# Kernel tuning notes

Hardware: AMD Instinct MI355X
Metric: run time of the kernel (lower is better)

## Reference

```python
import jax, jax.numpy as jnp
import numpy as np

OUT_F, IN_F, BLOCK, RANK = 8192, 8192, 32, 16
B, S = 4, 256
Q_ZERO = 128.0      # symmetric int8-style zero point for the Q8_0-like quants
LORA_SCALE = 2.0    # patch alpha applied by the patch function


def setup_inputs() -> dict:
    key = jax.random.key(0)
    k1, k2, k3, k4, k5, k6 = jax.random.split(key, 6)
    x = jax.random.normal(k1, (B, S, IN_F), dtype=jnp.float32)
    # block-quantized weight: int quants in [0,256) and per-block scales
    q_int = jax.random.randint(k2, (OUT_F, IN_F // BLOCK, BLOCK), 0, 256, dtype=jnp.int32)
    scales = jax.random.uniform(k3, (OUT_F, IN_F // BLOCK), dtype=jnp.float32) * 0.02
    lora_A = jax.random.normal(k4, (RANK, IN_F), dtype=jnp.float32) * 0.02
    lora_B = jax.random.normal(k5, (OUT_F, RANK), dtype=jnp.float32) * 0.02
    bias = jax.random.normal(k6, (OUT_F,), dtype=jnp.float32)
    return {"x": x, "q_int": q_int, "scales": scales,
            "lora_A": lora_A, "lora_B": lora_B, "bias": bias}


def reference(x, q_int, scales, lora_A, lora_B, bias):
    # --- get_weight(): dequantize GGML block-quantized tensor ---
    # w[o, b, e] = (q[o, b, e] - 128) * scale[o, b]
    w = (q_int.astype(jnp.float32) - Q_ZERO) * scales[:, :, None]   # [out, in//BLOCK, BLOCK]
    w = w.reshape(OUT_F, IN_F)                                      # [out, in]
    # --- apply patch function (LoRA add) ---
    w = w + LORA_SCALE * (lora_B @ lora_A)                          # [out, in]
    # --- cast_bias_weight + F.linear ---
    w = w.astype(x.dtype)
    y = jnp.einsum('bsi,oi->bso', x, w) + bias.astype(x.dtype)      # [B, S, out]
    return y
```

## Files before the change

### kernel.cpp

```cpp
#include <hip/hip_runtime.h>
#include <hip/hip_bf16.h>
#include <stdint.h>

#define OUT_F 8192
#define IN_F  8192
#define RANK  16
#define M_TOT 1024
#define BM 128
#define BN 128
#define BK 64
#define NK (IN_F / BK)
#define SCB (IN_F / 32)

typedef __bf16 bf16x8 __attribute__((ext_vector_type(8)));
typedef float  f32x4  __attribute__((ext_vector_type(4)));

static __device__ __forceinline__ uint32_t pack_bf16(float lo, float hi) {
    uint32_t a = __builtin_bit_cast(uint32_t, lo);
    uint32_t b = __builtin_bit_cast(uint32_t, hi);
    return ((a + 0x8000u) >> 16) | ((b + 0x8000u) & 0xffff0000u);
}

__global__ __launch_bounds__(256) void prep_kernel(
    const float* __restrict__ x, const int* __restrict__ q,
    uint2* __restrict__ xb2, uint32_t* __restrict__ qu32,
    float* __restrict__ t)
{
    const int gid = blockIdx.x * 256 + threadIdx.x;
    if (gid < M_TOT * RANK) t[gid] = 0.f;

    const float4* x4 = (const float4*)x;
#pragma unroll
    for (int j = 0; j < 4; ++j) {
        const int i = gid + j * 524288;
        const float4 v = x4[i];
        uint2 p;
        p.x = pack_bf16(v.x, v.y);
        p.y = pack_bf16(v.z, v.w);
        xb2[i] = p;
    }

    const int4* q4 = (const int4*)q;
#pragma unroll 8
    for (int k = 0; k < 32; ++k) {
        const size_t i = (size_t)gid + (size_t)k * 524288;
        const int4 a = q4[i];
        qu32[i] = (uint32_t)a.x | ((uint32_t)a.y << 8) |
                  ((uint32_t)a.z << 16) | ((uint32_t)a.w << 24);
    }
}

__global__ __launch_bounds__(256) void convert_kernel(
    const float* __restrict__ x, uint2* __restrict__ xb2, float* __restrict__ t)
{
    const int tid = threadIdx.x, b = blockIdx.x;
    if (b < 64) t[b * 256 + tid] = 0.f;
    const float4* x4 = (const float4*)x;
    const int base = b * 256 + tid;
#pragma unroll
    for (int j = 0; j < 8; ++j) {
        const int i = base + j * 262144;
        const float4 v = x4[i];
        uint2 p;
        p.x = pack_bf16(v.x, v.y);
        p.y = pack_bf16(v.z, v.w);
        xb2[i] = p;
    }
}

__global__ __launch_bounds__(256) void lora_t_kernel(
    const uint16_t* __restrict__ xb, const float* __restrict__ lora_A,
    float* __restrict__ t)
{
    const int b = blockIdx.x;
    const int mt = b >> 6, ks = b & 63;
    const int tid = threadIdx.x, wave = tid >> 6, lane = tid & 63;
    const int fr = lane & 15, quad = lane >> 4;
    const int m = mt * 64 + wave * 16 + fr;
    const int k0 = ks * 128 + quad * 8;

    f32x4 acc = {0.f, 0.f, 0.f, 0.f};
    const uint16_t* xr = xb + (size_t)m * IN_F + k0;
    const float* ar = lora_A + (size_t)fr * IN_F + k0;

#pragma unroll
    for (int s = 0; s < 4; ++s) {
        const bf16x8 af = *(const bf16x8*)(xr + s * 32);
        const float4 a0 = *(const float4*)(ar + s * 32);
        const float4 a1 = *(const float4*)(ar + s * 32 + 4);
        bf16x8 bfr;
        uint32_t* bp = (uint32_t*)&bfr;
        bp[0] = pack_bf16(a0.x, a0.y); bp[1] = pack_bf16(a0.z, a0.w);
        bp[2] = pack_bf16(a1.x, a1.y); bp[3] = pack_bf16(a1.z, a1.w);
        acc = __builtin_amdgcn_mfma_f32_16x16x32_bf16(af, bfr, acc, 0, 0, 0);
    }
    const int mout = mt * 64 + wave * 16 + quad * 4;
#pragma unroll
    for (int r = 0; r < 4; ++r)
        atomicAdd(&t[(size_t)(mout + r) * RANK + fr], acc[r]);
}

#define GEMM_STEP_U(KT, P, CUR, NXT)                                           \
    {                                                                          \
        const int ktn = ((KT) + 2) & (NK - 1);                                 \
        _Pragma("unroll")                                                      \
        for (int j = 0; j < 8; ++j) {                                          \
            const int row = qrow + 16 * j;                                     \
            qv[(P) ^ 1][j] = *(const uint32_t*)(qbase + (size_t)row * IN_F + ktn * BK); \
            sc[(P) ^ 1][j] = scales[(size_t)(n0 + row) * SCB + ktn * 2 + qhi]; \
        }                                                                      \
        const int kta = ((KT) + 1) & (NK - 1);                                 \
        _Pragma("unroll")                                                      \
        for (int i = 0; i < 4; ++i) {                                          \
            __builtin_amdgcn_global_load_lds(                                  \
                (const __attribute__((address_space(1))) uint32_t*)(xsrc + (size_t)kta * BK + (size_t)i * 8 * IN_F), \
                (__attribute__((address_space(3))) uint32_t*)(&xs[NXT][(wave * 32 + i * 8) * BK]), \
                16, 0, 0);                                                     \
        }                                                                      \
        _Pragma("unroll")                                                      \
        for (int j = 0; j < 8; ++j) {                                          \
            const float s = sc[P][j];                                          \
            const float c = -128.f * s;                                        \
            const uint32_t qq = qv[P][j];                                      \
            uint2 pk;                                                          \
            pk.x = pack_bf16(fmaf((float)(qq & 0xffu), s, c),                  \
                             fmaf((float)((qq >> 8) & 0xffu), s, c));          \
            pk.y = pack_bf16(fmaf((float)((qq >> 16) & 0xffu), s, c),          \
                             fmaf((float)(qq >> 24), s, c));                   \
            *(uint2*)(&wt[NXT][(qrow + 16 * j) * BK + wpos]) = pk;             \
        }                                                                      \
        _Pragma("unroll")                                                      \
        for (int kk = 0; kk < BK; kk += 32) {                                  \
            bf16x8 af[4], bfr[4];                                              \
            const int pp = (((kk >> 3) + quad) ^ (fr & 7)) * 8;                \
            _Pragma("unroll")                                                  \
            for (int i = 0; i < 4; ++i)                                        \
                af[i] = *(const bf16x8*)(&xs[CUR][(wm * 64 + i * 16 + fr) * BK + pp]); \
            _Pragma("unroll")                                                  \
            for (int j = 0; j < 4; ++j)                                        \
                bfr[j] = *(const bf16x8*)(&wt[CUR][(wn * 64 + j * 16 + fr) * BK + pp]); \
            _Pragma("unroll")                                                  \
            for (int i = 0; i < 4; ++i)                                        \
                _Pragma("unroll")                                              \
                for (int j = 0; j < 4; ++j)                                    \
                    acc[i][j] = __builtin_amdgcn_mfma_f32_16x16x32_bf16(af[i], bfr[j], acc[i][j], 0, 0, 0); \
        }                                                                      \
        __syncthreads();                                                       \
    }

__global__ __launch_bounds__(256, 2) void gemm_u8_kernel(
    const uint16_t* __restrict__ xb,
    const uint8_t*  __restrict__ qu8,
    const float*    __restrict__ scales,
    const float*    __restrict__ t,
    const float*    __restrict__ loraB,
    const float*    __restrict__ bias,
    float*          __restrict__ out)
{
    __shared__ __align__(16) uint16_t xs[2][BM * BK];
    __shared__ __align__(16) uint16_t wt[2][BN * BK];

    const int bx    = blockIdx.x;
    const int mtile = bx >> 6;
    const int ntile = bx & 63;
    const int m0 = mtile * BM;
    const int n0 = ntile * BN;

    const int tid  = threadIdx.x;
    const int wave = tid >> 6;
    const int lane = tid & 63;
    const int wm = wave & 1, wn = wave >> 1;
    const int fr = lane & 15;
    const int quad = lane >> 4;

    const int qrow  = tid >> 4;
    const int qcol4 = (tid & 15) * 4;
    const int qhi   = (tid >> 3) & 1;
    const int wpos = ((((tid >> 1) & 7) ^ (qrow & 7)) * 8) + (tid & 1) * 4;

    const uint8_t* qbase = qu8 + (size_t)n0 * IN_F + qcol4;

    f32x4 acc[4][4];
    const f32x4 z = {0.f, 0.f, 0.f, 0.f};
#pragma unroll
    for (int i = 0; i < 4; ++i)
#pragma unroll
        for (int j = 0; j < 4; ++j) acc[i][j] = z;

    uint32_t qv[2][8];
    float    sc[2][8];

#pragma unroll
    for (int j = 0; j < 8; ++j) {
        const int row = qrow + 16 * j;
        qv[0][j] = *(const uint32_t*)(qbase + (size_t)row * IN_F);
        sc[0][j] = scales[(size_t)(n0 + row) * SCB + qhi];
    }

    {
        if (tid < 128) {
            const int row = tid, s = row & 7;
            const float4* tp = (const float4*)(t + (size_t)(m0 + row) * RANK);
            const float4 v0 = tp[0], v1 = tp[1], v2 = tp[2], v3 = tp[3];
            uint32_t vals[8];
            vals[0] = pack_bf16(v0.x, v0.y); vals[1] = pack_bf16(v0.z, v0.w);
            vals[2] = pack_bf16(v1.x, v1.y); vals[3] = pack_bf16(v1.z, v1.w);
            vals[4] = pack_bf16(v2.x, v2.y); vals[5] = pack_bf16(v2.z, v2.w);
            vals[6] = pack_bf16(v3.x, v3.y); vals[7] = pack_bf16(v3.z, v3.w);
            uint32_t* dst = (uint32_t*)(&xs[0][row * BK]);
#pragma unroll
            for (int c = 0; c < 8; ++c) {
                const int p = (c ^ s) * 4;
                if (c < 2) {
                    dst[p + 0] = vals[c * 4 + 0]; dst[p + 1] = vals[c * 4 + 1];
                    dst[p + 2] = vals[c * 4 + 2]; dst[p + 3] = vals[c * 4 + 3];
                } else {
                    dst[p + 0] = 0; dst[p + 1] = 0; dst[p + 2] = 0; dst[p + 3] = 0;
                }
            }
        } else {
            const int row = tid - 128, s = row & 7;
            const float4* bp = (const float4*)(loraB + (size_t)(n0 + row) * RANK);
            const float4 v0 = bp[0], v1 = bp[1], v2 = bp[2], v3 = bp[3];
            uint32_t vals[8];
            vals[0] = pack_bf16(2.f * v0.x, 2.f * v0.y); vals[1] = pack_bf16(2.f * v0.z, 2.f * v0.w);
            vals[2] = pack_bf16(2.f * v1.x, 2.f * v1.y); vals[3] = pack_bf16(2.f * v1.z, 2.f * v1.w);
            vals[4] = pack_bf16(2.f * v2.x, 2.f * v2.y); vals[5] = pack_bf16(2.f * v2.z, 2.f * v2.w);
            vals[6] = pack_bf16(2.f * v3.x, 2.f * v3.y); vals[7] = pack_bf16(2.f * v3.z, 2.f * v3.w);
            uint32_t* dst = (uint32_t*)(&wt[0][row * BK]);
#pragma unroll
            for (int c = 0; c < 8; ++c) {
                const int p = (c ^ s) * 4;
                if (c < 2) {
                    dst[p + 0] = vals[c * 4 + 0]; dst[p + 1] = vals[c * 4 + 1];
                    dst[p + 2] = vals[c * 4 + 2]; dst[p + 3] = vals[c * 4 + 3];
                } else {
                    dst[p + 0] = 0; dst[p + 1] = 0; dst[p + 2] = 0; dst[p + 3] = 0;
                }
            }
        }
        __syncthreads();
        const int pp = (quad ^ (fr & 7)) * 8;
        bf16x8 af[4], bfr[4];
#pragma unroll
        for (int i = 0; i < 4; ++i)
            af[i] = *(const bf16x8*)(&xs[0][(wm * 64 + i * 16 + fr) * BK + pp]);
#pragma unroll
        for (int j = 0; j < 4; ++j)
            bfr[j] = *(const bf16x8*)(&wt[0][(wn * 64 + j * 16 + fr) * BK + pp]);
#pragma unroll
        for (int i = 0; i < 4; ++i)
#pragma unroll
            for (int j = 0; j < 4; ++j)
                acc[i][j] = __builtin_amdgcn_mfma_f32_16x16x32_bf16(af[i], bfr[j], acc[i][j], 0, 0, 0);
        __syncthreads();
    }

    const int xrow   = wave * 32 + (lane >> 3);
    const int xchunk = (lane & 7) ^ (lane >> 3);
    const uint16_t* xsrc = xb + (size_t)(m0 + xrow) * IN_F + xchunk * 8;

#pragma unroll
    for (int i = 0; i < 4; ++i) {
        __builtin_amdgcn_global_load_lds(
            (const __attribute__((address_space(1))) uint32_t*)(xsrc + (size_t)i * 8 * IN_F),
            (__attribute__((address_space(3))) uint32_t*)(&xs[0][(wave * 32 + i * 8) * BK]),
            16, 0, 0);
    }
#pragma unroll
    for (int j = 0; j < 8; ++j) {
        const float s = sc[0][j];
        const float c = -128.f * s;
        const uint32_t qq = qv[0][j];
        uint2 pk;
        pk.x = pack_bf16(fmaf((float)(qq & 0xffu), s, c),
                         fmaf((float)((qq >> 8) & 0xffu), s, c));
        pk.y = pack_bf16(fmaf((float)((qq >> 16) & 0xffu), s, c),
                         fmaf((float)(qq >> 24), s, c));
        *(uint2*)(&wt[0][(qrow + 16 * j) * BK + wpos]) = pk;
    }
#pragma unroll
    for (int j = 0; j < 8; ++j) {
        const int row = qrow + 16 * j;
        qv[0][j] = *(const uint32_t*)(qbase + (size_t)row * IN_F + 1 * BK);
        sc[0][j] = scales[(size_t)(n0 + row) * SCB + 2 + qhi];
    }
    __syncthreads();

    for (int kt = 0; kt < NK; kt += 2) {
        GEMM_STEP_U(kt,     0, 0, 1);
        GEMM_STEP_U(kt + 1, 1, 1, 0);
    }

#pragma unroll
    for (int j = 0; j < 4; ++j) {
        const int col = n0 + wn * 64 + j * 16 + fr;
        const float bv = bias[col];
#pragma unroll
        for (int i = 0; i < 4; ++i) {
            const int rbase = m0 + wm * 64 + i * 16 + quad * 4;
#pragma unroll
            for (int r = 0; r < 4; ++r)
                out[(size_t)(rbase + r) * OUT_F + col] = acc[i][j][r] + bv;
        }
    }
}

#define GEMM_STEP_L(KT, P, CUR, NXT)                                           \
    {                                                                          \
        const int ktn = ((KT) + 2) & (NK - 1);                                 \
        _Pragma("unroll")                                                      \
        for (int j = 0; j < 8; ++j) {                                          \
            const int row = qrow + 16 * j;                                     \
            qv[(P) ^ 1][j] = *(const int4*)(qbase + (size_t)row * IN_F + ktn * BK); \
            sc[(P) ^ 1][j] = scales[(size_t)(n0 + row) * SCB + ktn * 2 + qhi]; \
        }                                                                      \
        const int kta = ((KT) + 1) & (NK - 1);                                 \
        _Pragma("unroll")                                                      \
        for (int i = 0; i < 4; ++i) {                                          \
            __builtin_amdgcn_global_load_lds(                                  \
                (const __attribute__((address_space(1))) uint32_t*)(xsrc + (size_t)kta * BK + (size_t)i * 8 * IN_F), \
                (__attribute__((address_space(3))) uint32_t*)(&xs[NXT][(wave * 32 + i * 8) * BK]), \
                16, 0, 0);                                                     \
        }                                                                      \
        _Pragma("unroll")                                                      \
        for (int j = 0; j < 8; ++j) {                                          \
            const float s = sc[P][j];                                          \
            const float c = -128.f * s;                                        \
            const int4 qq = qv[P][j];                                          \
            uint2 pk;                                                          \
            pk.x = pack_bf16(fmaf((float)qq.x, s, c), fmaf((float)qq.y, s, c)); \
            pk.y = pack_bf16(fmaf((float)qq.z, s, c), fmaf((float)qq.w, s, c)); \
            *(uint2*)(&wt[NXT][(qrow + 16 * j) * BK + wpos]) = pk;             \
        }                                                                      \
        _Pragma("unroll")                                                      \
        for (int kk = 0; kk < BK; kk += 32) {                                  \
            bf16x8 af[4], bfr[4];                                              \
            const int pp = (((kk >> 3) + quad) ^ (fr & 7)) * 8;                \
            _Pragma("unroll")                                                  \
            for (int i = 0; i < 4; ++i)                                        \
                af[i] = *(const bf16x8*)(&xs[CUR][(wm * 64 + i * 16 + fr) * BK + pp]); \
            _Pragma("unroll")                                                  \
            for (int j = 0; j < 4; ++j)                                        \
                bfr[j] = *(const bf16x8*)(&wt[CUR][(wn * 64 + j * 16 + fr) * BK + pp]); \
            _Pragma("unroll")                                                  \
            for (int i = 0; i < 4; ++i)                                        \
                _Pragma("unroll")                                              \
                for (int j = 0; j < 4; ++j)                                    \
                    acc[i][j] = __builtin_amdgcn_mfma_f32_16x16x32_bf16(af[i], bfr[j], acc[i][j], 0, 0, 0); \
        }                                                                      \
        __syncthreads();                                                       \
    }

__global__ __launch_bounds__(256, 2) void gemm_kernel(
    const uint16_t* __restrict__ xb,
    const int*      __restrict__ q,
    const float*    __restrict__ scales,
    const float*    __restrict__ t,
    const float*    __restrict__ loraB,
    const float*    __restrict__ bias,
    float*          __restrict__ out)
{
    __shared__ __align__(16) uint16_t xs[2][BM * BK];
    __shared__ __align__(16) uint16_t wt[2][BN * BK];

    const int bx    = blockIdx.x;
    const int mtile = bx >> 6;
    const int ntile = bx & 63;
    const int m0 = mtile * BM;
    const int n0 = ntile * BN;

    const int tid  = threadIdx.x;
    const int wave = tid >> 6;
    const int lane = tid & 63;
    const int wm = wave & 1, wn = wave >> 1;
    const int fr = lane & 15;
    const int quad = lane >> 4;

    const int qrow  = tid >> 4;
    const int qcol4 = (tid & 15) * 4;
    const int qhi   = (tid >> 3) & 1;
    const int wpos = ((((tid >> 1) & 7) ^ (qrow & 7)) * 8) + (tid & 1) * 4;

    const int* qbase = q + (size_t)n0 * IN_F + qcol4;

    f32x4 acc[4][4];
    const f32x4 z = {0.f, 0.f, 0.f, 0.f};
#pragma unroll
    for (int i = 0; i < 4; ++i)
#pragma unroll
        for (int j = 0; j < 4; ++j) acc[i][j] = z;

    int4  qv[2][8];
    float sc[2][8];

#pragma unroll
    for (int j = 0; j < 8; ++j) {
        const int row = qrow + 16 * j;
        qv[0][j] = *(const int4*)(qbase + (size_t)row * IN_F);
        sc[0][j] = scales[(size_t)(n0 + row) * SCB + qhi];
    }

    {
        if (tid < 128) {
            const int row = tid, s = row & 7;
            const float4* tp = (const float4*)(t + (size_t)(m0 + row) * RANK);
            const float4 v0 = tp[0], v1 = tp[1], v2 = tp[2], v3 = tp[3];
            uint32_t vals[8];
            vals[0] = pack_bf16(v0.x, v0.y); vals[1] = pack_bf16(v0.z, v0.w);
            vals[2] = pack_bf16(v1.x, v1.y); vals[3] = pack_bf16(v1.z, v1.w);
            vals[4] = pack_bf16(v2.x, v2.y); vals[5] = pack_bf16(v2.z, v2.w);
            vals[6] = pack_bf16(v3.x, v3.y); vals[7] = pack_bf16(v3.z, v3.w);
            uint32_t* dst = (uint32_t*)(&xs[0][row * BK]);
#pragma unroll
            for (int c = 0; c < 8; ++c) {
                const int p = (c ^ s) * 4;
                if (c < 2) {
                    dst[p + 0] = vals[c * 4 + 0]; dst[p + 1] = vals[c * 4 + 1];
                    dst[p + 2] = vals[c * 4 + 2]; dst[p + 3] = vals[c * 4 + 3];
                } else {
                    dst[p + 0] = 0; dst[p + 1] = 0; dst[p + 2] = 0; dst[p + 3] = 0;
                }
            }
        } else {
            const int row = tid - 128, s = row & 7;
            const float4* bp = (const float4*)(loraB + (size_t)(n0 + row) * RANK);
            const float4 v0 = bp[0], v1 = bp[1], v2 = bp[2], v3 = bp[3];
            uint32_t vals[8];
            vals[0] = pack_bf16(2.f * v0.x, 2.f * v0.y); vals[1] = pack_bf16(2.f * v0.z, 2.f * v0.w);
            vals[2] = pack_bf16(2.f * v1.x, 2.f * v1.y); vals[3] = pack_bf16(2.f * v1.z, 2.f * v1.w);
            vals[4] = pack_bf16(2.f * v2.x, 2.f * v2.y); vals[5] = pack_bf16(2.f * v2.z, 2.f * v2.w);
            vals[6] = pack_bf16(2.f * v3.x, 2.f * v3.y); vals[7] = pack_bf16(2.f * v3.z, 2.f * v3.w);
            uint32_t* dst = (uint32_t*)(&wt[0][row * BK]);
#pragma unroll
            for (int c = 0; c < 8; ++c) {
                const int p = (c ^ s) * 4;
                if (c < 2) {
                    dst[p + 0] = vals[c * 4 + 0]; dst[p + 1] = vals[c * 4 + 1];
                    dst[p + 2] = vals[c * 4 + 2]; dst[p + 3] = vals[c * 4 + 3];
                } else {
                    dst[p + 0] = 0; dst[p + 1] = 0; dst[p + 2] = 0; dst[p + 3] = 0;
                }
            }
        }
        __syncthreads();
        const int pp = (quad ^ (fr & 7)) * 8;
        bf16x8 af[4], bfr[4];
#pragma unroll
        for (int i = 0; i < 4; ++i)
            af[i] = *(const bf16x8*)(&xs[0][(wm * 64 + i * 16 + fr) * BK + pp]);
#pragma unroll
        for (int j = 0; j < 4; ++j)
            bfr[j] = *(const bf16x8*)(&wt[0][(wn * 64 + j * 16 + fr) * BK + pp]);
#pragma unroll
        for (int i = 0; i < 4; ++i)
#pragma unroll
            for (int j = 0; j < 4; ++j)
                acc[i][j] = __builtin_amdgcn_mfma_f32_16x16x32_bf16(af[i], bfr[j], acc[i][j], 0, 0, 0);
        __syncthreads();
    }

    const int xrow   = wave * 32 + (lane >> 3);
    const int xchunk = (lane & 7) ^ (lane >> 3);
    const uint16_t* xsrc = xb + (size_t)(m0 + xrow) * IN_F + xchunk * 8;

#pragma unroll
    for (int i = 0; i < 4; ++i) {
        __builtin_amdgcn_global_load_lds(
            (const __attribute__((address_space(1))) uint32_t*)(xsrc + (size_t)i * 8 * IN_F),
            (__attribute__((address_space(3))) uint32_t*)(&xs[0][(wave * 32 + i * 8) * BK]),
            16, 0, 0);
    }
#pragma unroll
    for (int j = 0; j < 8; ++j) {
        const float s = sc[0][j];
        const float c = -128.f * s;
        const int4 qq = qv[0][j];
        uint2 pk;
        pk.x = pack_bf16(fmaf((float)qq.x, s, c), fmaf((float)qq.y, s, c));
        pk.y = pack_bf16(fmaf((float)qq.z, s, c), fmaf((float)qq.w, s, c));
        *(uint2*)(&wt[0][(qrow + 16 * j) * BK + wpos]) = pk;
    }
#pragma unroll
    for (int j = 0; j < 8; ++j) {
        const int row = qrow + 16 * j;
        qv[0][j] = *(const int4*)(qbase + (size_t)row * IN_F + 1 * BK);
        sc[0][j] = scales[(size_t)(n0 + row) * SCB + 2 + qhi];
    }
    __syncthreads();

    for (int kt = 0; kt < NK; kt += 2) {
        GEMM_STEP_L(kt,     0, 0, 1);
        GEMM_STEP_L(kt + 1, 1, 1, 0);
    }

#pragma unroll
    for (int j = 0; j < 4; ++j) {
        const int col = n0 + wn * 64 + j * 16 + fr;
        const float bv = bias[col];
#pragma unroll
        for (int i = 0; i < 4; ++i) {
            const int rbase = m0 + wm * 64 + i * 16 + quad * 4;
#pragma unroll
            for (int r = 0; r < 4; ++r)
                out[(size_t)(rbase + r) * OUT_F + col] = acc[i][j][r] + bv;
        }
    }
}

extern "C" void kernel_launch(void* const* d_in, const int* in_sizes, int n_in,
                              void* d_out, int out_size, void* d_ws, size_t ws_size,
                              hipStream_t stream) {
    const float* x      = (const float*)d_in[0];
    const int*   q      = (const int*)d_in[1];
    const float* scales = (const float*)d_in[2];
    const float* lora_A = (const float*)d_in[3];
    const float* lora_B = (const float*)d_in[4];
    const float* bias   = (const float*)d_in[5];
    float* out = (float*)d_out;

    const size_t xb_bytes = (size_t)M_TOT * IN_F * sizeof(uint16_t);
    const size_t t_bytes  = (size_t)M_TOT * RANK * sizeof(float);
    const size_t q8_off   = xb_bytes + t_bytes;
    const size_t q8_bytes = (size_t)OUT_F * IN_F;

    uint16_t* xb = (uint16_t*)d_ws;
    float*    t  = (float*)((char*)d_ws + xb_bytes);

    if (ws_size >= q8_off + q8_bytes) {
        uint8_t* qu8 = (uint8_t*)d_ws + q8_off;
        prep_kernel<<<2048, 256, 0, stream>>>(x, q, (uint2*)xb, (uint32_t*)qu8, t);
        lora_t_kernel<<<1024, 256, 0, stream>>>(xb, lora_A, t);
        gemm_u8_kernel<<<(M_TOT / BM) * (OUT_F / BN), 256, 0, stream>>>(
            xb, qu8, scales, t, lora_B, bias, out);
    } else {
        convert_kernel<<<M_TOT, 256, 0, stream>>>(x, (uint2*)xb, t);
        lora_t_kernel<<<1024, 256, 0, stream>>>(xb, lora_A, t);
        gemm_kernel<<<(M_TOT / BM) * (OUT_F / BN), 256, 0, stream>>>(
            xb, q, scales, t, lora_B, bias, out);
    }
}
```

Baseline: 602.3 us.

## Dequantize weights to bf16 in prep kernel and stream them via LDS DMA

Adds a prep kernel that fully dequantizes the int32 quants with their scales into a bf16 weight matrix in workspace. A new GEMM kernel then loads both the x and W tiles with global_load_lds, so the per-tile dequant ALU work and register-staged stores to LDS drop out of the main loop. In exchange the prep pass writes a 128 MB bf16 weight and the GEMM reads 2 bytes per weight instead of 1. This path is used only when the workspace is large enough, otherwise the uint8 and int32 paths remain as fallbacks.

```diff
diff --git a/kernel.cpp b/kernel.cpp
--- a/kernel.cpp
+++ b/kernel.cpp
@@ -19,6 +19,43 @@
     uint32_t a = __builtin_bit_cast(uint32_t, lo);
     uint32_t b = __builtin_bit_cast(uint32_t, hi);
     return ((a + 0x8000u) >> 16) | ((b + 0x8000u) & 0xffff0000u);
+}
+
+__global__ __launch_bounds__(256) void prep_w_kernel(
+    const float* __restrict__ x, const int* __restrict__ q,
+    const float* __restrict__ scales,
+    uint2* __restrict__ xb2, uint4* __restrict__ wb4,
+    float* __restrict__ t)
+{
+    const int gid = blockIdx.x * 256 + threadIdx.x;
+    if (gid < M_TOT * RANK) t[gid] = 0.f;
+
+    const float4* x4 = (const float4*)x;
+#pragma unroll
+    for (int j = 0; j < 4; ++j) {
+        const int i = gid + j * 524288;
+        const float4 v = x4[i];
+        uint2 p;
+        p.x = pack_bf16(v.x, v.y);
+        p.y = pack_bf16(v.z, v.w);
+        xb2[i] = p;
+    }
+
+    const int4* q4 = (const int4*)q;
+#pragma unroll 4
+    for (int sweep = 0; sweep < 16; ++sweep) {
+        const size_t i8 = (size_t)gid + (size_t)sweep * 524288;
+        const float s = scales[(i8 * 8) >> 5];
+        const float c = -128.f * s;
+        const int4 a = q4[i8 * 2];
+        const int4 b = q4[i8 * 2 + 1];
+        uint4 o;
+        o.x = pack_bf16(fmaf((float)a.x, s, c), fmaf((float)a.y, s, c));
+        o.y = pack_bf16(fmaf((float)a.z, s, c), fmaf((float)a.w, s, c));
+        o.z = pack_bf16(fmaf((float)b.x, s, c), fmaf((float)b.y, s, c));
+        o.w = pack_bf16(fmaf((float)b.z, s, c), fmaf((float)b.w, s, c));
+        wb4[i8] = o;
+    }
 }
 
 __global__ __launch_bounds__(256) void prep_kernel(
@@ -100,15 +137,8 @@
         atomicAdd(&t[(size_t)(mout + r) * RANK + fr], acc[r]);
 }
 
-#define GEMM_STEP_U(KT, P, CUR, NXT)                                           \
+#define GEMM_STEP_W(KT, CUR, NXT)                                              \
     {                                                                          \
-        const int ktn = ((KT) + 2) & (NK - 1);                                 \
-        _Pragma("unroll")                                                      \
-        for (int j = 0; j < 8; ++j) {                                          \
-            const int row = qrow + 16 * j;                                     \
-            qv[(P) ^ 1][j] = *(const uint32_t*)(qbase + (size_t)row * IN_F + ktn * BK); \
-            sc[(P) ^ 1][j] = scales[(size_t)(n0 + row) * SCB + ktn * 2 + qhi]; \
-        }                                                                      \
         const int kta = ((KT) + 1) & (NK - 1);                                 \
         _Pragma("unroll")                                                      \
         for (int i = 0; i < 4; ++i) {                                          \
@@ -116,18 +146,10 @@
                 (const __attribute__((address_space(1))) uint32_t*)(xsrc + (size_t)kta * BK + (size_t)i * 8 * IN_F), \
                 (__attribute__((address_space(3))) uint32_t*)(&xs[NXT][(wave * 32 + i * 8) * BK]), \
                 16, 0, 0);                                                     \
-        }                                                                      \
-        _Pragma("unroll")                                                      \
-        for (int j = 0; j < 8; ++j) {                                          \
-            const float s = sc[P][j];                                          \
-            const float c = -128.f * s;                                        \
-            const uint32_t qq = qv[P][j];                                      \
-            uint2 pk;                                                          \
-            pk.x = pack_bf16(fmaf((float)(qq & 0xffu), s, c),                  \
-                             fmaf((float)((qq >> 8) & 0xffu), s, c));          \
-            pk.y = pack_bf16(fmaf((float)((qq >> 16) & 0xffu), s, c),          \
-                             fmaf((float)(qq >> 24), s, c));                   \
-            *(uint2*)(&wt[NXT][(qrow + 16 * j) * BK + wpos]) = pk;             \
+            __builtin_amdgcn_global_load_lds(                                  \
+                (const __attribute__((address_space(1))) uint32_t*)(wsrc + (size_t)kta * BK + (size_t)i * 8 * IN_F), \
+                (__attribute__((address_space(3))) uint32_t*)(&wt[NXT][(wave * 32 + i * 8) * BK]), \
+                16, 0, 0);                                                     \
         }                                                                      \
         _Pragma("unroll")                                                      \
         for (int kk = 0; kk < BK; kk += 32) {                                  \
@@ -148,10 +170,9 @@
         __syncthreads();                                                       \
     }
 
-__global__ __launch_bounds__(256, 2) void gemm_u8_kernel(
+__global__ __launch_bounds__(256, 2) void gemm_w_kernel(
     const uint16_t* __restrict__ xb,
-    const uint8_t*  __restrict__ qu8,
-    const float*    __restrict__ scales,
+    const uint16_t* __restrict__ wb,
     const float*    __restrict__ t,
     const float*    __restrict__ loraB,
     const float*    __restrict__ bias,
@@ -173,29 +194,12 @@
     const int fr = lane & 15;
     const int quad = lane >> 4;
 
-    const int qrow  = tid >> 4;
-    const int qcol4 = (tid & 15) * 4;
-    const int qhi   = (tid >> 3) & 1;
-    const int wpos = ((((tid >> 1) & 7) ^ (qrow & 7)) * 8) + (tid & 1) * 4;
-
-    const uint8_t* qbase = qu8 + (size_t)n0 * IN_F + qcol4;
-
     f32x4 acc[4][4];
     const f32x4 z = {0.f, 0.f, 0.f, 0.f};
 #pragma unroll
     for (int i = 0; i < 4; ++i)
 #pragma unroll
         for (int j = 0; j < 4; ++j) acc[i][j] = z;
-
-    uint32_t qv[2][8];
-    float    sc[2][8];
-
-#pragma unroll
-    for (int j = 0; j < 8; ++j) {
-        const int row = qrow + 16 * j;
-        qv[0][j] = *(const uint32_t*)(qbase + (size_t)row * IN_F);
-        sc[0][j] = scales[(size_t)(n0 + row) * SCB + qhi];
-    }
 
     {
         if (tid < 128) {
@@ -256,9 +260,10 @@
         __syncthreads();
     }
 
-    const int xrow   = wave * 32 + (lane >> 3);
-    const int xchunk = (lane & 7) ^ (lane >> 3);
-    const uint16_t* xsrc = xb + (size_t)(m0 + xrow) * IN_F + xchunk * 8;
+    const int srow   = wave * 32 + (lane >> 3);
+    const int schunk = (lane & 7) ^ (lane >> 3);
+    const uint16_t* xsrc = xb + (size_t)(m0 + srow) * IN_F + schunk * 8;
+    const uint16_t* wsrc = wb + (size_t)(n0 + srow) * IN_F + schunk * 8;
 
 #pragma unroll
     for (int i = 0; i < 4; ++i) {
@@ -266,30 +271,16 @@
             (const __attribute__((address_space(1))) uint32_t*)(xsrc + (size_t)i * 8 * IN_F),
             (__attribute__((address_space(3))) uint32_t*)(&xs[0][(wave * 32 + i * 8) * BK]),
             16, 0, 0);
-    }
-#pragma unroll
-    for (int j = 0; j < 8; ++j) {
-        const float s = sc[0][j];
-        const float c = -128.f * s;
-        const uint32_t qq = qv[0][j];
-        uint2 pk;
-        pk.x = pack_bf16(fmaf((float)(qq & 0xffu), s, c),
-                         fmaf((float)((qq >> 8) & 0xffu), s, c));
-        pk.y = pack_bf16(fmaf((float)((qq >> 16) & 0xffu), s, c),
-                         fmaf((float)(qq >> 24), s, c));
-        *(uint2*)(&wt[0][(qrow + 16 * j) * BK + wpos]) = pk;
-    }
-#pragma unroll
-    for (int j = 0; j < 8; ++j) {
-        const int row = qrow + 16 * j;
-        qv[0][j] = *(const uint32_t*)(qbase + (size_t)row * IN_F + 1 * BK);
-        sc[0][j] = scales[(size_t)(n0 + row) * SCB + 2 + qhi];
+        __builtin_amdgcn_global_load_lds(
+            (const __attribute__((address_space(1))) uint32_t*)(wsrc + (size_t)i * 8 * IN_F),
+            (__attribute__((address_space(3))) uint32_t*)(&wt[0][(wave * 32 + i * 8) * BK]),
+            16, 0, 0);
     }
     __syncthreads();
 
     for (int kt = 0; kt < NK; kt += 2) {
-        GEMM_STEP_U(kt,     0, 0, 1);
-        GEMM_STEP_U(kt + 1, 1, 1, 0);
+        GEMM_STEP_W(kt,     0, 1);
+        GEMM_STEP_W(kt + 1, 1, 0);
     }
 
 #pragma unroll
@@ -306,13 +297,13 @@
     }
 }
 
-#define GEMM_STEP_L(KT, P, CUR, NXT)                                           \
+#define GEMM_STEP_U(KT, P, CUR, NXT)                                           \
     {                                                                          \
         const int ktn = ((KT) + 2) & (NK - 1);                                 \
         _Pragma("unroll")                                                      \
         for (int j = 0; j < 8; ++j) {                                          \
             const int row = qrow + 16 * j;                                     \
-            qv[(P) ^ 1][j] = *(const int4*)(qbase + (size_t)row * IN_F + ktn * BK); \
+            qv[(P) ^ 1][j] = *(const uint32_t*)(qbase + (size_t)row * IN_F + ktn * BK); \
             sc[(P) ^ 1][j] = scales[(size_t)(n0 + row) * SCB + ktn * 2 + qhi]; \
         }                                                                      \
         const int kta = ((KT) + 1) & (NK - 1);                                 \
@@ -327,10 +318,12 @@
         for (int j = 0; j < 8; ++j) {                                          \
             const float s = sc[P][j];                                          \
             const float c = -128.f * s;                                        \
-            const int4 qq = qv[P][j];                                          \
+            const uint32_t qq = qv[P][j];                                      \
             uint2 pk;                                                          \
-            pk.x = pack_bf16(fmaf((float)qq.x, s, c), fmaf((float)qq.y, s, c)); \
-            pk.y = pack_bf16(fmaf((float)qq.z, s, c), fmaf((float)qq.w, s, c)); \
+            pk.x = pack_bf16(fmaf((float)(qq & 0xffu), s, c),                  \
+                             fmaf((float)((qq >> 8) & 0xffu), s, c));          \
+            pk.y = pack_bf16(fmaf((float)((qq >> 16) & 0xffu), s, c),          \
+                             fmaf((float)(qq >> 24), s, c));                   \
             *(uint2*)(&wt[NXT][(qrow + 16 * j) * BK + wpos]) = pk;             \
         }                                                                      \
         _Pragma("unroll")                                                      \
@@ -352,9 +345,9 @@
         __syncthreads();                                                       \
     }
 
-__global__ __launch_bounds__(256, 2) void gemm_kernel(
+__global__ __launch_bounds__(256, 2) void gemm_u8_kernel(
     const uint16_t* __restrict__ xb,
-    const int*      __restrict__ q,
+    const uint8_t*  __restrict__ qu8,
     const float*    __restrict__ scales,
     const float*    __restrict__ t,
     const float*    __restrict__ loraB,
@@ -382,7 +375,7 @@
     const int qhi   = (tid >> 3) & 1;
     const int wpos = ((((tid >> 1) & 7) ^ (qrow & 7)) * 8) + (tid & 1) * 4;
 
-    const int* qbase = q + (size_t)n0 * IN_F + qcol4;
+    const uint8_t* qbase = qu8 + (size_t)n0 * IN_F + qcol4;
 
     f32x4 acc[4][4];
     const f32x4 z = {0.f, 0.f, 0.f, 0.f};
@@ -391,13 +384,13 @@
 #pragma unroll
         for (int j = 0; j < 4; ++j) acc[i][j] = z;
 
-    int4  qv[2][8];
-    float sc[2][8];
+    uint32_t qv[2][8];
+    float    sc[2][8];
 
 #pragma unroll
     for (int j = 0; j < 8; ++j) {
         const int row = qrow + 16 * j;
-        qv[0][j] = *(const int4*)(qbase + (size_t)row * IN_F);
+        qv[0][j] = *(const uint32_t*)(qbase + (size_t)row * IN_F);
         sc[0][j] = scales[(size_t)(n0 + row) * SCB + qhi];
     }
 
@@ -475,6 +468,210 @@
     for (int j = 0; j < 8; ++j) {
         const float s = sc[0][j];
         const float c = -128.f * s;
+        const uint32_t qq = qv[0][j];
+        uint2 pk;
+        pk.x = pack_bf16(fmaf((float)(qq & 0xffu), s, c),
+                         fmaf((float)((qq >> 8) & 0xffu), s, c));
+        pk.y = pack_bf16(fmaf((float)((qq >> 16) & 0xffu), s, c),
+                         fmaf((float)(qq >> 24), s, c));
+        *(uint2*)(&wt[0][(qrow + 16 * j) * BK + wpos]) = pk;
+    }
+#pragma unroll
+    for (int j = 0; j < 8; ++j) {
+        const int row = qrow + 16 * j;
+        qv[0][j] = *(const uint32_t*)(qbase + (size_t)row * IN_F + 1 * BK);
+        sc[0][j] = scales[(size_t)(n0 + row) * SCB + 2 + qhi];
+    }
+    __syncthreads();
+
+    for (int kt = 0; kt < NK; kt += 2) {
+        GEMM_STEP_U(kt,     0, 0, 1);
+        GEMM_STEP_U(kt + 1, 1, 1, 0);
+    }
+
+#pragma unroll
+    for (int j = 0; j < 4; ++j) {
+        const int col = n0 + wn * 64 + j * 16 + fr;
+        const float bv = bias[col];
+#pragma unroll
+        for (int i = 0; i < 4; ++i) {
+            const int rbase = m0 + wm * 64 + i * 16 + quad * 4;
+#pragma unroll
+            for (int r = 0; r < 4; ++r)
+                out[(size_t)(rbase + r) * OUT_F + col] = acc[i][j][r] + bv;
+        }
+    }
+}
+
+#define GEMM_STEP_L(KT, P, CUR, NXT)                                           \
+    {                                                                          \
+        const int ktn = ((KT) + 2) & (NK - 1);                                 \
+        _Pragma("unroll")                                                      \
+        for (int j = 0; j < 8; ++j) {                                          \
+            const int row = qrow + 16 * j;                                     \
+            qv[(P) ^ 1][j] = *(const int4*)(qbase + (size_t)row * IN_F + ktn * BK); \
+            sc[(P) ^ 1][j] = scales[(size_t)(n0 + row) * SCB + ktn * 2 + qhi]; \
+        }                                                                      \
+        const int kta = ((KT) + 1) & (NK - 1);                                 \
+        _Pragma("unroll")                                                      \
+        for (int i = 0; i < 4; ++i) {                                          \
+            __builtin_amdgcn_global_load_lds(                                  \
+                (const __attribute__((address_space(1))) uint32_t*)(xsrc + (size_t)kta * BK + (size_t)i * 8 * IN_F), \
+                (__attribute__((address_space(3))) uint32_t*)(&xs[NXT][(wave * 32 + i * 8) * BK]), \
+                16, 0, 0);                                                     \
+        }                                                                      \
+        _Pragma("unroll")                                                      \
+        for (int j = 0; j < 8; ++j) {                                          \
+            const float s = sc[P][j];                                          \
+            const float c = -128.f * s;                                        \
+            const int4 qq = qv[P][j];                                          \
+            uint2 pk;                                                          \
+            pk.x = pack_bf16(fmaf((float)qq.x, s, c), fmaf((float)qq.y, s, c)); \
+            pk.y = pack_bf16(fmaf((float)qq.z, s, c), fmaf((float)qq.w, s, c)); \
+            *(uint2*)(&wt[NXT][(qrow + 16 * j) * BK + wpos]) = pk;             \
+        }                                                                      \
+        _Pragma("unroll")                                                      \
+        for (int kk = 0; kk < BK; kk += 32) {                                  \
+            bf16x8 af[4], bfr[4];                                              \
+            const int pp = (((kk >> 3) + quad) ^ (fr & 7)) * 8;                \
+            _Pragma("unroll")                                                  \
+            for (int i = 0; i < 4; ++i)                                        \
+                af[i] = *(const bf16x8*)(&xs[CUR][(wm * 64 + i * 16 + fr) * BK + pp]); \
+            _Pragma("unroll")                                                  \
+            for (int j = 0; j < 4; ++j)                                        \
+                bfr[j] = *(const bf16x8*)(&wt[CUR][(wn * 64 + j * 16 + fr) * BK + pp]); \
+            _Pragma("unroll")                                                  \
+            for (int i = 0; i < 4; ++i)                                        \
+                _Pragma("unroll")                                              \
+                for (int j = 0; j < 4; ++j)                                    \
+                    acc[i][j] = __builtin_amdgcn_mfma_f32_16x16x32_bf16(af[i], bfr[j], acc[i][j], 0, 0, 0); \
+        }                                                                      \
+        __syncthreads();                                                       \
+    }
+
+__global__ __launch_bounds__(256, 2) void gemm_kernel(
+    const uint16_t* __restrict__ xb,
+    const int*      __restrict__ q,
+    const float*    __restrict__ scales,
+    const float*    __restrict__ t,
+    const float*    __restrict__ loraB,
+    const float*    __restrict__ bias,
+    float*          __restrict__ out)
+{
+    __shared__ __align__(16) uint16_t xs[2][BM * BK];
+    __shared__ __align__(16) uint16_t wt[2][BN * BK];
+
+    const int bx    = blockIdx.x;
+    const int mtile = bx >> 6;
+    const int ntile = bx & 63;
+    const int m0 = mtile * BM;
+    const int n0 = ntile * BN;
+
+    const int tid  = threadIdx.x;
+    const int wave = tid >> 6;
+    const int lane = tid & 63;
+    const int wm = wave & 1, wn = wave >> 1;
+    const int fr = lane & 15;
+    const int quad = lane >> 4;
+
+    const int qrow  = tid >> 4;
+    const int qcol4 = (tid & 15) * 4;
+    const int qhi   = (tid >> 3) & 1;
+    const int wpos = ((((tid >> 1) & 7) ^ (qrow & 7)) * 8) + (tid & 1) * 4;
+
+    const int* qbase = q + (size_t)n0 * IN_F + qcol4;
+
+    f32x4 acc[4][4];
+    const f32x4 z = {0.f, 0.f, 0.f, 0.f};
+#pragma unroll
+    for (int i = 0; i < 4; ++i)
+#pragma unroll
+        for (int j = 0; j < 4; ++j) acc[i][j] = z;
+
+    int4  qv[2][8];
+    float sc[2][8];
+
+#pragma unroll
+    for (int j = 0; j < 8; ++j) {
+        const int row = qrow + 16 * j;
+        qv[0][j] = *(const int4*)(qbase + (size_t)row * IN_F);
+        sc[0][j] = scales[(size_t)(n0 + row) * SCB + qhi];
+    }
+
+    {
+        if (tid < 128) {
+            const int row = tid, s = row & 7;
+            const float4* tp = (const float4*)(t + (size_t)(m0 + row) * RANK);
+            const float4 v0 = tp[0], v1 = tp[1], v2 = tp[2], v3 = tp[3];
+            uint32_t vals[8];
+            vals[0] = pack_bf16(v0.x, v0.y); vals[1] = pack_bf16(v0.z, v0.w);
+            vals[2] = pack_bf16(v1.x, v1.y); vals[3] = pack_bf16(v1.z, v1.w);
+            vals[4] = pack_bf16(v2.x, v2.y); vals[5] = pack_bf16(v2.z, v2.w);
+            vals[6] = pack_bf16(v3.x, v3.y); vals[7] = pack_bf16(v3.z, v3.w);
+            uint32_t* dst = (uint32_t*)(&xs[0][row * BK]);
+#pragma unroll
+            for (int c = 0; c < 8; ++c) {
+                const int p = (c ^ s) * 4;
+                if (c < 2) {
+                    dst[p + 0] = vals[c * 4 + 0]; dst[p + 1] = vals[c * 4 + 1];
+                    dst[p + 2] = vals[c * 4 + 2]; dst[p + 3] = vals[c * 4 + 3];
+                } else {
+                    dst[p + 0] = 0; dst[p + 1] = 0; dst[p + 2] = 0; dst[p + 3] = 0;
+                }
+            }
+        } else {
+            const int row = tid - 128, s = row & 7;
+            const float4* bp = (const float4*)(loraB + (size_t)(n0 + row) * RANK);
+            const float4 v0 = bp[0], v1 = bp[1], v2 = bp[2], v3 = bp[3];
+            uint32_t vals[8];
+            vals[0] = pack_bf16(2.f * v0.x, 2.f * v0.y); vals[1] = pack_bf16(2.f * v0.z, 2.f * v0.w);
+            vals[2] = pack_bf16(2.f * v1.x, 2.f * v1.y); vals[3] = pack_bf16(2.f * v1.z, 2.f * v1.w);
+            vals[4] = pack_bf16(2.f * v2.x, 2.f * v2.y); vals[5] = pack_bf16(2.f * v2.z, 2.f * v2.w);
+            vals[6] = pack_bf16(2.f * v3.x, 2.f * v3.y); vals[7] = pack_bf16(2.f * v3.z, 2.f * v3.w);
+            uint32_t* dst = (uint32_t*)(&wt[0][row * BK]);
+#pragma unroll
+            for (int c = 0; c < 8; ++c) {
+                const int p = (c ^ s) * 4;
+                if (c < 2) {
+                    dst[p + 0] = vals[c * 4 + 0]; dst[p + 1] = vals[c * 4 + 1];
+                    dst[p + 2] = vals[c * 4 + 2]; dst[p + 3] = vals[c * 4 + 3];
+                } else {
+                    dst[p + 0] = 0; dst[p + 1] = 0; dst[p + 2] = 0; dst[p + 3] = 0;
+                }
+            }
+        }
+        __syncthreads();
+        const int pp = (quad ^ (fr & 7)) * 8;
+        bf16x8 af[4], bfr[4];
+#pragma unroll
+        for (int i = 0; i < 4; ++i)
+            af[i] = *(const bf16x8*)(&xs[0][(wm * 64 + i * 16 + fr) * BK + pp]);
+#pragma unroll
+        for (int j = 0; j < 4; ++j)
+            bfr[j] = *(const bf16x8*)(&wt[0][(wn * 64 + j * 16 + fr) * BK + pp]);
+#pragma unroll
+        for (int i = 0; i < 4; ++i)
+#pragma unroll
+            for (int j = 0; j < 4; ++j)
+                acc[i][j] = __builtin_amdgcn_mfma_f32_16x16x32_bf16(af[i], bfr[j], acc[i][j], 0, 0, 0);
+        __syncthreads();
+    }
+
+    const int xrow   = wave * 32 + (lane >> 3);
+    const int xchunk = (lane & 7) ^ (lane >> 3);
+    const uint16_t* xsrc = xb + (size_t)(m0 + xrow) * IN_F + xchunk * 8;
+
+#pragma unroll
+    for (int i = 0; i < 4; ++i) {
+        __builtin_amdgcn_global_load_lds(
+            (const __attribute__((address_space(1))) uint32_t*)(xsrc + (size_t)i * 8 * IN_F),
+            (__attribute__((address_space(3))) uint32_t*)(&xs[0][(wave * 32 + i * 8) * BK]),
+            16, 0, 0);
+    }
+#pragma unroll
+    for (int j = 0; j < 8; ++j) {
+        const float s = sc[0][j];
+        const float c = -128.f * s;
         const int4 qq = qv[0][j];
         uint2 pk;
         pk.x = pack_bf16(fmaf((float)qq.x, s, c), fmaf((float)qq.y, s, c));
@@ -521,14 +718,22 @@
 
     const size_t xb_bytes = (size_t)M_TOT * IN_F * sizeof(uint16_t);
     const size_t t_bytes  = (size_t)M_TOT * RANK * sizeof(float);
-    const size_t q8_off   = xb_bytes + t_bytes;
+    const size_t big_off  = xb_bytes + t_bytes;
+    const size_t w_bytes  = (size_t)OUT_F * IN_F * 2;
     const size_t q8_bytes = (size_t)OUT_F * IN_F;
 
     uint16_t* xb = (uint16_t*)d_ws;
     float*    t  = (float*)((char*)d_ws + xb_bytes);
 
-    if (ws_size >= q8_off + q8_bytes) {
-        uint8_t* qu8 = (uint8_t*)d_ws + q8_off;
+    if (ws_size >= big_off + w_bytes) {
+        uint16_t* wb = (uint16_t*)((char*)d_ws + big_off);
+        prep_w_kernel<<<2048, 256, 0, stream>>>(
+            x, q, scales, (uint2*)xb, (uint4*)wb, t);
+        lora_t_kernel<<<1024, 256, 0, stream>>>(xb, lora_A, t);
+        gemm_w_kernel<<<(M_TOT / BM) * (OUT_F / BN), 256, 0, stream>>>(
+            xb, wb, t, lora_B, bias, out);
+    } else if (ws_size >= big_off + q8_bytes) {
+        uint8_t* qu8 = (uint8_t*)d_ws + big_off;
         prep_kernel<<<2048, 256, 0, stream>>>(x, q, (uint2*)xb, (uint32_t*)qu8, t);
         lora_t_kernel<<<1024, 256, 0, stream>>>(xb, lora_A, t);
         gemm_u8_kernel<<<(M_TOT / BM) * (OUT_F / BN), 256, 0, stream>>>(
```

Result: slower. 625.2 us (+3.8%).
